# Performance work log

Hardware: AMD Instinct MI355X
Metric: run time of the kernel (lower is better)

Reference implementation:

```python
import jax, jax.numpy as jnp
import numpy as np

N_NODES = 100000
N_EDGES = 1600000
IN_DIM = 128
HID_DIM = 128


def _gcn_conv(x, edge_index, W, b, num_nodes):
    h = x @ W  # [N, H]
    loops = jnp.arange(num_nodes, dtype=edge_index.dtype)
    src = jnp.concatenate([edge_index[0], loops])  # [E+N]
    dst = jnp.concatenate([edge_index[1], loops])
    deg = jax.ops.segment_sum(jnp.ones_like(dst, dtype=h.dtype), dst,
                              num_segments=num_nodes)  # [N], >=1 due to self-loops
    inv_sqrt_deg = jax.lax.rsqrt(deg)
    norm = inv_sqrt_deg[src] * inv_sqrt_deg[dst]  # [E+N]
    msgs = h[src] * norm[:, None]  # gather + scale, [E+N, H]
    out = jax.ops.segment_sum(msgs, dst, num_segments=num_nodes)  # scatter-add
    return out + b


def setup_inputs() -> dict:
    key = jax.random.key(0)
    k1, k2, k3, k4, k5 = jax.random.split(key, 5)
    x = jax.random.normal(k1, (N_NODES, IN_DIM), dtype=jnp.float32)
    edge_index = jax.random.randint(k2, (2, N_EDGES), 0, N_NODES, dtype=jnp.int64)
    s1 = 1.0 / np.sqrt(IN_DIM)
    s2 = 1.0 / np.sqrt(HID_DIM)
    W1 = jax.random.uniform(k3, (IN_DIM, HID_DIM), jnp.float32, -s1, s1)
    W2 = jax.random.uniform(k4, (HID_DIM, HID_DIM), jnp.float32, -s2, s2)
    b1 = jnp.zeros((HID_DIM,), jnp.float32)
    b2 = jnp.zeros((HID_DIM,), jnp.float32)
    return {"x": x, "edge_index": edge_index, "W1": W1, "b1": b1, "W2": W2, "b2": b2}


def reference(x, edge_index, W1, b1, W2, b2):
    n = x.shape[0]
    h = _gcn_conv(x, edge_index, W1, b1, n)
    h = jax.nn.relu(h)
    h = _gcn_conv(h, edge_index, W2, b2, n)
    return h.mean(axis=0)  # [HID_DIM]
```

## Files before the change

### kernel.cpp

```cpp
#include <hip/hip_runtime.h>

#define TPB 256

typedef unsigned int uint32;
typedef float float4v __attribute__((ext_vector_type(4)));
typedef unsigned int uint4v __attribute__((ext_vector_type(4)));

static __device__ __forceinline__ unsigned short f2bf(float f) {
  unsigned int u = __float_as_uint(f);
  unsigned int r = (u + 0x7FFFu + ((u >> 16) & 1u)) >> 16;
  return (unsigned short)r;
}
static __device__ __forceinline__ float bf_lo(uint32 v) {
  return __uint_as_float(v << 16);
}
static __device__ __forceinline__ float bf_hi(uint32 v) {
  return __uint_as_float(v & 0xFFFF0000u);
}

static __device__ __forceinline__ int edge_val(const int* __restrict__ ep,
                                               long long idx, int is64) {
  return is64 ? ep[2 * idx] : ep[idx];
}

__global__ void k_detect(const int* __restrict__ ep, long long E,
                         int* __restrict__ flag) {
  int lim = (E < 16384) ? (int)E : 16384;
  int found = 0;
  for (int i = threadIdx.x; i < lim; i += TPB) found |= (ep[2 * i + 1] != 0);
  if (found) atomicOr(flag, 1);
}

__global__ void k_count(const int* __restrict__ ep, long long E,
                        const int* __restrict__ flag, int* __restrict__ deg) {
  int is64 = (*flag == 0);
  long long stride = (long long)gridDim.x * blockDim.x;
  for (long long e = blockIdx.x * (long long)blockDim.x + threadIdx.x; e < E;
       e += stride) {
    int d = edge_val(ep, E + e, is64);
    atomicAdd(&deg[d], 1);
  }
}

__global__ void k_bsum(const int* __restrict__ deg, int N,
                       int* __restrict__ bsums) {
  __shared__ int lds[TPB];
  int t = threadIdx.x;
  int i = blockIdx.x * TPB + t;
  lds[t] = (i < N) ? deg[i] : 0;
  __syncthreads();
  for (int off = TPB / 2; off > 0; off >>= 1) {
    if (t < off) lds[t] += lds[t + off];
    __syncthreads();
  }
  if (t == 0) bsums[blockIdx.x] = lds[0];
}

__global__ void k_bscan(int* __restrict__ bsums, int nb) {
  __shared__ int lds[512];
  int t = threadIdx.x;
  int v = (t < nb) ? bsums[t] : 0;
  lds[t] = v;
  __syncthreads();
  for (int off = 1; off < 512; off <<= 1) {
    int x = (t >= off) ? lds[t - off] : 0;
    __syncthreads();
    lds[t] += x;
    __syncthreads();
  }
  if (t < nb) bsums[t] = lds[t] - v;
}

__global__ void k_scan3(const int* __restrict__ deg, const int* __restrict__ bsums,
                        int N, int* __restrict__ row_start, int* __restrict__ cursor,
                        float* __restrict__ r) {
  __shared__ int lds[TPB];
  int t = threadIdx.x;
  int i = blockIdx.x * TPB + t;
  int v = (i < N) ? deg[i] : 0;
  lds[t] = v;
  __syncthreads();
  for (int off = 1; off < TPB; off <<= 1) {
    int x = (t >= off) ? lds[t - off] : 0;
    __syncthreads();
    lds[t] += x;
    __syncthreads();
  }
  if (i < N) {
    int ex = lds[t] - v + bsums[blockIdx.x];
    row_start[i] = ex;
    cursor[i] = ex;
    r[i] = rsqrtf((float)(v + 1));
  }
}

__global__ void k_fill(const int* __restrict__ ep, long long E,
                       const int* __restrict__ flag, int* __restrict__ cursor,
                       int* __restrict__ csr_src) {
  int is64 = (*flag == 0);
  long long stride = (long long)gridDim.x * blockDim.x;
  for (long long e = blockIdx.x * (long long)blockDim.x + threadIdx.x; e < E;
       e += stride) {
    int s = edge_val(ep, e, is64);
    int d = edge_val(ep, E + e, is64);
    int pos = atomicAdd(&cursor[d], 1);
    csr_src[pos] = s;
  }
}

template <int XBF>
__global__ __launch_bounds__(TPB, 4) void k_gemm(
    const void* __restrict__ Xv, const float* __restrict__ W,
    const float* __restrict__ r, unsigned short* __restrict__ outB, int N) {
  __shared__ uint32 wl[128 * 64];
  for (int i = threadIdx.x; i < 128 * 64; i += TPB) {
    int k = i >> 6, p = i & 63;
    float2 wv = *reinterpret_cast<const float2*>(&W[k * 128 + p * 2]);
    wl[i] = (uint32)f2bf(wv.x) | ((uint32)f2bf(wv.y) << 16);
  }
  __syncthreads();
  int wave = threadIdx.x >> 6, lane = threadIdx.x & 63;
  int row0 = (blockIdx.x * 4 + wave) * 8;
  if (row0 >= N) return;
  const int c0 = lane * 2;
  float2 acc[8];
#pragma unroll
  for (int q = 0; q < 8; q++) acc[q] = make_float2(0.f, 0.f);

  if (XBF == 0) {
    const float* X = (const float*)Xv;
    for (int kk = 0; kk < 128; kk += 4) {
      float4v xv[8];
#pragma unroll
      for (int q = 0; q < 8; q++) {
        int rr = row0 + q;
        if (rr >= N) rr = N - 1;
        xv[q] = __builtin_nontemporal_load(
            reinterpret_cast<const float4v*>(&X[(size_t)rr * 128 + kk]));
      }
#pragma unroll
      for (int u = 0; u < 4; u++) {
        uint32 wv = wl[(kk + u) * 64 + lane];
        float wx = bf_lo(wv), wy = bf_hi(wv);
#pragma unroll
        for (int q = 0; q < 8; q++) {
          float xk = xv[q][u];
          acc[q].x = fmaf(xk, wx, acc[q].x);
          acc[q].y = fmaf(xk, wy, acc[q].y);
        }
      }
    }
  } else {
    const unsigned short* X = (const unsigned short*)Xv;
    for (int kk = 0; kk < 128; kk += 8) {
      uint4v xv[8];
#pragma unroll
      for (int q = 0; q < 8; q++) {
        int rr = row0 + q;
        if (rr >= N) rr = N - 1;
        xv[q] = *reinterpret_cast<const uint4v*>(&X[(size_t)rr * 128 + kk]);
      }
#pragma unroll
      for (int u = 0; u < 8; u++) {
        uint32 wv = wl[(kk + u) * 64 + lane];
        float wx = bf_lo(wv), wy = bf_hi(wv);
#pragma unroll
        for (int q = 0; q < 8; q++) {
          uint32 xw = xv[q][u >> 1];
          float xk = (u & 1) ? bf_hi(xw) : bf_lo(xw);
          acc[q].x = fmaf(xk, wx, acc[q].x);
          acc[q].y = fmaf(xk, wy, acc[q].y);
        }
      }
    }
  }
#pragma unroll
  for (int q = 0; q < 8; q++) {
    int rr = row0 + q;
    if (rr < N) {
      float sc = r[rr];
      uint32 o = (uint32)f2bf(acc[q].x * sc) | ((uint32)f2bf(acc[q].y * sc) << 16);
      *reinterpret_cast<uint32*>(&outB[(size_t)rr * 128 + c0]) = o;
    }
  }
}

template <int RELU, int COLSUM>
__global__ __launch_bounds__(TPB) void k_agg(
    const unsigned short* __restrict__ HsB, const float* __restrict__ r,
    const int* __restrict__ row_start, const int* __restrict__ deg,
    const int* __restrict__ csr_src, const float* __restrict__ bias,
    unsigned short* __restrict__ outB, float* __restrict__ colsum, int N) {
  __shared__ float red[4][128];
  int wave = threadIdx.x >> 6, lane = threadIdx.x & 63;
  int gw = blockIdx.x * 4 + wave, nw = gridDim.x * 4;
  const int c0 = lane * 2;
  float2 b = *reinterpret_cast<const float2*>(&bias[c0]);
  float2 csum = make_float2(0.f, 0.f);

  for (int i0 = gw; i0 < N; i0 += 2 * nw) {
    const int iA = i0;
    const int iB = i0 + nw;
    const int hasB = (iB < N);
    int sA = __builtin_amdgcn_readfirstlane(row_start[iA]);
    int dA = __builtin_amdgcn_readfirstlane(deg[iA]);
    int sB = 0, dB = 0;
    if (hasB) {
      sB = __builtin_amdgcn_readfirstlane(row_start[iB]);
      dB = __builtin_amdgcn_readfirstlane(deg[iB]);
    }
    uint32 selfA = *reinterpret_cast<const uint32*>(&HsB[(size_t)iA * 128 + c0]);
    float2 aA = make_float2(bf_lo(selfA), bf_hi(selfA));
    float2 aB = make_float2(0.f, 0.f);
    if (hasB) {
      uint32 selfB = *reinterpret_cast<const uint32*>(&HsB[(size_t)iB * 128 + c0]);
      aB = make_float2(bf_lo(selfB), bf_hi(selfB));
    }
    int jA = 0, jB = 0;
    while (jA + 8 <= dA && jB + 8 <= dB) {
      int ia[8], ib[8];
#pragma unroll
      for (int u = 0; u < 8; u++) ia[u] = csr_src[sA + jA + u];
#pragma unroll
      for (int u = 0; u < 8; u++) ib[u] = csr_src[sB + jB + u];
      uint32 va[8], vb[8];
#pragma unroll
      for (int u = 0; u < 8; u++)
        va[u] = *reinterpret_cast<const uint32*>(&HsB[(size_t)ia[u] * 128 + c0]);
#pragma unroll
      for (int u = 0; u < 8; u++)
        vb[u] = *reinterpret_cast<const uint32*>(&HsB[(size_t)ib[u] * 128 + c0]);
#pragma unroll
      for (int u = 0; u < 8; u++) {
        aA.x += bf_lo(va[u]); aA.y += bf_hi(va[u]);
        aB.x += bf_lo(vb[u]); aB.y += bf_hi(vb[u]);
      }
      jA += 8; jB += 8;
    }
    while (jA + 8 <= dA) {
      int ia[8];
#pragma unroll
      for (int u = 0; u < 8; u++) ia[u] = csr_src[sA + jA + u];
      uint32 va[8];
#pragma unroll
      for (int u = 0; u < 8; u++)
        va[u] = *reinterpret_cast<const uint32*>(&HsB[(size_t)ia[u] * 128 + c0]);
#pragma unroll
      for (int u = 0; u < 8; u++) { aA.x += bf_lo(va[u]); aA.y += bf_hi(va[u]); }
      jA += 8;
    }
    while (jB + 8 <= dB) {
      int ib[8];
#pragma unroll
      for (int u = 0; u < 8; u++) ib[u] = csr_src[sB + jB + u];
      uint32 vb[8];
#pragma unroll
      for (int u = 0; u < 8; u++)
        vb[u] = *reinterpret_cast<const uint32*>(&HsB[(size_t)ib[u] * 128 + c0]);
#pragma unroll
      for (int u = 0; u < 8; u++) { aB.x += bf_lo(vb[u]); aB.y += bf_hi(vb[u]); }
      jB += 8;
    }
    if (jA + 4 <= dA && jB + 4 <= dB) {
      int ia[4], ib[4];
#pragma unroll
      for (int u = 0; u < 4; u++) ia[u] = csr_src[sA + jA + u];
#pragma unroll
      for (int u = 0; u < 4; u++) ib[u] = csr_src[sB + jB + u];
      uint32 va[4], vb[4];
#pragma unroll
      for (int u = 0; u < 4; u++)
        va[u] = *reinterpret_cast<const uint32*>(&HsB[(size_t)ia[u] * 128 + c0]);
#pragma unroll
      for (int u = 0; u < 4; u++)
        vb[u] = *reinterpret_cast<const uint32*>(&HsB[(size_t)ib[u] * 128 + c0]);
#pragma unroll
      for (int u = 0; u < 4; u++) {
        aA.x += bf_lo(va[u]); aA.y += bf_hi(va[u]);
        aB.x += bf_lo(vb[u]); aB.y += bf_hi(vb[u]);
      }
      jA += 4; jB += 4;
    }
    if (jA + 4 <= dA) {
      int ia[4];
#pragma unroll
      for (int u = 0; u < 4; u++) ia[u] = csr_src[sA + jA + u];
      uint32 va[4];
#pragma unroll
      for (int u = 0; u < 4; u++)
        va[u] = *reinterpret_cast<const uint32*>(&HsB[(size_t)ia[u] * 128 + c0]);
#pragma unroll
      for (int u = 0; u < 4; u++) { aA.x += bf_lo(va[u]); aA.y += bf_hi(va[u]); }
      jA += 4;
    }
    if (jB + 4 <= dB) {
      int ib[4];
#pragma unroll
      for (int u = 0; u < 4; u++) ib[u] = csr_src[sB + jB + u];
      uint32 vb[4];
#pragma unroll
      for (int u = 0; u < 4; u++)
        vb[u] = *reinterpret_cast<const uint32*>(&HsB[(size_t)ib[u] * 128 + c0]);
#pragma unroll
      for (int u = 0; u < 4; u++) { aB.x += bf_lo(vb[u]); aB.y += bf_hi(vb[u]); }
      jB += 4;
    }
    for (; jA < dA && jB < dB; jA++, jB++) {
      int s0 = csr_src[sA + jA], s1 = csr_src[sB + jB];
      uint32 v0 = *reinterpret_cast<const uint32*>(&HsB[(size_t)s0 * 128 + c0]);
      uint32 v1 = *reinterpret_cast<const uint32*>(&HsB[(size_t)s1 * 128 + c0]);
      aA.x += bf_lo(v0); aA.y += bf_hi(v0);
      aB.x += bf_lo(v1); aB.y += bf_hi(v1);
    }
    for (; jA < dA; jA++) {
      int s0 = csr_src[sA + jA];
      uint32 v0 = *reinterpret_cast<const uint32*>(&HsB[(size_t)s0 * 128 + c0]);
      aA.x += bf_lo(v0); aA.y += bf_hi(v0);
    }
    for (; jB < dB; jB++) {
      int s1 = csr_src[sB + jB];
      uint32 v1 = *reinterpret_cast<const uint32*>(&HsB[(size_t)s1 * 128 + c0]);
      aB.x += bf_lo(v1); aB.y += bf_hi(v1);
    }
    {
      float ri = r[iA];
      float v0 = fmaf(ri, aA.x, b.x), v1 = fmaf(ri, aA.y, b.y);
      if (RELU) { v0 = fmaxf(v0, 0.f); v1 = fmaxf(v1, 0.f); }
      if (COLSUM) {
        csum.x += v0; csum.y += v1;
      } else {
        uint32 o = (uint32)f2bf(v0) | ((uint32)f2bf(v1) << 16);
        __builtin_nontemporal_store(
            o, reinterpret_cast<uint32*>(&outB[(size_t)iA * 128 + c0]));
      }
    }
    if (hasB) {
      float ri = r[iB];
      float v0 = fmaf(ri, aB.x, b.x), v1 = fmaf(ri, aB.y, b.y);
      if (RELU) { v0 = fmaxf(v0, 0.f); v1 = fmaxf(v1, 0.f); }
      if (COLSUM) {
        csum.x += v0; csum.y += v1;
      } else {
        uint32 o = (uint32)f2bf(v0) | ((uint32)f2bf(v1) << 16);
        __builtin_nontemporal_store(
            o, reinterpret_cast<uint32*>(&outB[(size_t)iB * 128 + c0]));
      }
    }
  }
  if (COLSUM) {
    red[wave][c0] = csum.x;
    red[wave][c0 + 1] = csum.y;
    __syncthreads();
    if (wave == 0) {
      float sx = red[0][c0] + red[1][c0] + red[2][c0] + red[3][c0];
      float sy = red[0][c0 + 1] + red[1][c0 + 1] + red[2][c0 + 1] + red[3][c0 + 1];
      atomicAdd(&colsum[c0], sx);
      atomicAdd(&colsum[c0 + 1], sy);
    }
  }
}

__global__ void k_final(const float* __restrict__ colsum, float* __restrict__ out,
                        float invN) {
  int c = threadIdx.x;
  out[c] = colsum[c] * invN;
}

extern "C" void kernel_launch(void* const* d_in, const int* in_sizes, int n_in,
                              void* d_out, int out_size, void* d_ws, size_t ws_size,
                              hipStream_t stream) {
  const float* x = (const float*)d_in[0];
  const int* ep = (const int*)d_in[1];
  const float* W1 = (const float*)d_in[2];
  const float* b1 = (const float*)d_in[3];
  const float* W2 = (const float*)d_in[4];
  const float* b2 = (const float*)d_in[5];
  float* outp = (float*)d_out;

  const int N = in_sizes[0] / 128;
  const long long E = in_sizes[1] / 2;

  char* ws = (char*)d_ws;
  size_t off = 0;
  auto carve = [&](size_t bytes) -> void* {
    void* p = ws + off;
    off = (off + bytes + 255) & ~(size_t)255;
    return p;
  };
  unsigned short* HsB = (unsigned short*)carve((size_t)N * 128 * 2);
  unsigned short* YB = (unsigned short*)carve((size_t)N * 128 * 2);
  float* rr = (float*)carve((size_t)N * 4);
  int* deg = (int*)carve((size_t)N * 4);
  int* rs = (int*)carve((size_t)N * 4);
  int* cur = (int*)carve((size_t)N * 4);
  int* csr = (int*)carve((size_t)E * 4);
  int* bsums = (int*)carve(4096 * 4);
  int* flag = (int*)carve(256);
  float* colsum = (float*)carve(512);

  hipMemsetAsync(flag, 0, 4, stream);
  hipMemsetAsync(deg, 0, (size_t)N * 4, stream);
  hipMemsetAsync(colsum, 0, 512, stream);

  k_detect<<<1, TPB, 0, stream>>>(ep, E, flag);
  k_count<<<2048, TPB, 0, stream>>>(ep, E, flag, deg);
  int nb = (N + TPB - 1) / TPB;
  k_bsum<<<nb, TPB, 0, stream>>>(deg, N, bsums);
  k_bscan<<<1, 512, 0, stream>>>(bsums, nb);
  k_scan3<<<nb, TPB, 0, stream>>>(deg, bsums, N, rs, cur, rr);
  k_fill<<<2048, TPB, 0, stream>>>(ep, E, flag, cur, csr);

  int gblocks = (N + 31) / 32;
  k_gemm<0><<<gblocks, TPB, 0, stream>>>(x, W1, rr, HsB, N);
  k_agg<1, 0><<<2048, TPB, 0, stream>>>(HsB, rr, rs, deg, csr, b1, YB, nullptr, N);
  k_gemm<1><<<gblocks, TPB, 0, stream>>>(YB, W2, rr, HsB, N);
  k_agg<0, 1><<<2048, TPB, 0, stream>>>(HsB, rr, rs, deg, csr, b2, nullptr, colsum, N);
  k_final<<<1, 128, 0, stream>>>(colsum, outp, 1.0f / (float)N);
}
```

Baseline: 744.0 us.

## Fuse second-layer GEMM into first aggregation kernel epilogue

The layer-1 aggregation kernel now multiplies each finished row by W2, held as bf16 in shared memory, and writes the scaled layer-2 features directly. This removes the separate second GEMM launch and the bf16 round trip of the intermediate activations. The cost is a per-row 128x128 matvec done by one wave through LDS, which is less efficient than a tiled GEMM and adds 32KB of LDS per block, which can lower occupancy of the latency-bound gather. It also splits the aggregation into two specialized kernels and makes the CSR fill use nontemporal stores.

New measurement: 997.6 us. +34.1%, slower.

```diff
diff --git a/kernel.cpp b/kernel.cpp
--- a/kernel.cpp
+++ b/kernel.cpp
@@ -104,13 +104,12 @@
     int s = edge_val(ep, e, is64);
     int d = edge_val(ep, E + e, is64);
     int pos = atomicAdd(&cursor[d], 1);
-    csr_src[pos] = s;
-  }
-}
-
-template <int XBF>
+    __builtin_nontemporal_store(s, &csr_src[pos]);
+  }
+}
+
 __global__ __launch_bounds__(TPB, 4) void k_gemm(
-    const void* __restrict__ Xv, const float* __restrict__ W,
+    const float* __restrict__ X, const float* __restrict__ W,
     const float* __restrict__ r, unsigned short* __restrict__ outB, int N) {
   __shared__ uint32 wl[128 * 64];
   for (int i = threadIdx.x; i < 128 * 64; i += TPB) {
@@ -126,51 +125,24 @@
   float2 acc[8];
 #pragma unroll
   for (int q = 0; q < 8; q++) acc[q] = make_float2(0.f, 0.f);
-
-  if (XBF == 0) {
-    const float* X = (const float*)Xv;
-    for (int kk = 0; kk < 128; kk += 4) {
-      float4v xv[8];
+  for (int kk = 0; kk < 128; kk += 4) {
+    float4v xv[8];
+#pragma unroll
+    for (int q = 0; q < 8; q++) {
+      int rr = row0 + q;
+      if (rr >= N) rr = N - 1;
+      xv[q] = __builtin_nontemporal_load(
+          reinterpret_cast<const float4v*>(&X[(size_t)rr * 128 + kk]));
+    }
+#pragma unroll
+    for (int u = 0; u < 4; u++) {
+      uint32 wv = wl[(kk + u) * 64 + lane];
+      float wx = bf_lo(wv), wy = bf_hi(wv);
 #pragma unroll
       for (int q = 0; q < 8; q++) {
-        int rr = row0 + q;
-        if (rr >= N) rr = N - 1;
-        xv[q] = __builtin_nontemporal_load(
-            reinterpret_cast<const float4v*>(&X[(size_t)rr * 128 + kk]));
-      }
-#pragma unroll
-      for (int u = 0; u < 4; u++) {
-        uint32 wv = wl[(kk + u) * 64 + lane];
-        float wx = bf_lo(wv), wy = bf_hi(wv);
-#pragma unroll
-        for (int q = 0; q < 8; q++) {
-          float xk = xv[q][u];
-          acc[q].x = fmaf(xk, wx, acc[q].x);
-          acc[q].y = fmaf(xk, wy, acc[q].y);
-        }
-      }
-    }
-  } else {
-    const unsigned short* X = (const unsigned short*)Xv;
-    for (int kk = 0; kk < 128; kk += 8) {
-      uint4v xv[8];
-#pragma unroll
-      for (int q = 0; q < 8; q++) {
-        int rr = row0 + q;
-        if (rr >= N) rr = N - 1;
-        xv[q] = *reinterpret_cast<const uint4v*>(&X[(size_t)rr * 128 + kk]);
-      }
-#pragma unroll
-      for (int u = 0; u < 8; u++) {
-        uint32 wv = wl[(kk + u) * 64 + lane];
-        float wx = bf_lo(wv), wy = bf_hi(wv);
-#pragma unroll
-        for (int q = 0; q < 8; q++) {
-          uint32 xw = xv[q][u >> 1];
-          float xk = (u & 1) ? bf_hi(xw) : bf_lo(xw);
-          acc[q].x = fmaf(xk, wx, acc[q].x);
-          acc[q].y = fmaf(xk, wy, acc[q].y);
-        }
+        float xk = xv[q][u];
+        acc[q].x = fmaf(xk, wx, acc[q].x);
+        acc[q].y = fmaf(xk, wy, acc[q].y);
       }
     }
   }
@@ -185,18 +157,43 @@
   }
 }
 
-template <int RELU, int COLSUM>
-__global__ __launch_bounds__(TPB) void k_agg(
+static __device__ __forceinline__ void y_to_hs2(
+    float v0, float v1, float ri, int i, int wave, int lane, int c0,
+    const uint32* __restrict__ w2l, float* __restrict__ yrow,
+    unsigned short* __restrict__ outB) {
+  float* yw = yrow + wave * 128;
+  *reinterpret_cast<float2*>(&yw[lane * 2]) = make_float2(v0, v1);
+  float hx = 0.f, hy = 0.f;
+  for (int k4 = 0; k4 < 32; k4++) {
+    float4v y4 = *reinterpret_cast<const float4v*>(&yw[k4 * 4]);
+#pragma unroll
+    for (int j = 0; j < 4; j++) {
+      uint32 wv = w2l[(k4 * 4 + j) * 64 + lane];
+      hx = fmaf(y4[j], bf_lo(wv), hx);
+      hy = fmaf(y4[j], bf_hi(wv), hy);
+    }
+  }
+  uint32 o = (uint32)f2bf(hx * ri) | ((uint32)f2bf(hy * ri) << 16);
+  *reinterpret_cast<uint32*>(&outB[(size_t)i * 128 + c0]) = o;
+}
+
+__global__ __launch_bounds__(TPB) void k_aggF(
     const unsigned short* __restrict__ HsB, const float* __restrict__ r,
     const int* __restrict__ row_start, const int* __restrict__ deg,
     const int* __restrict__ csr_src, const float* __restrict__ bias,
-    unsigned short* __restrict__ outB, float* __restrict__ colsum, int N) {
-  __shared__ float red[4][128];
+    const float* __restrict__ W2, unsigned short* __restrict__ outB, int N) {
+  __shared__ uint32 w2l[128 * 64];
+  __shared__ float yrow[4 * 128];
+  for (int i = threadIdx.x; i < 128 * 64; i += TPB) {
+    int k = i >> 6, p = i & 63;
+    float2 wv = *reinterpret_cast<const float2*>(&W2[k * 128 + p * 2]);
+    w2l[i] = (uint32)f2bf(wv.x) | ((uint32)f2bf(wv.y) << 16);
+  }
+  __syncthreads();
   int wave = threadIdx.x >> 6, lane = threadIdx.x & 63;
   int gw = blockIdx.x * 4 + wave, nw = gridDim.x * 4;
   const int c0 = lane * 2;
   float2 b = *reinterpret_cast<const float2*>(&bias[c0]);
-  float2 csum = make_float2(0.f, 0.f);
 
   for (int i0 = gw; i0 < N; i0 += 2 * nw) {
     const int iA = i0;
@@ -325,38 +322,173 @@
     {
       float ri = r[iA];
       float v0 = fmaf(ri, aA.x, b.x), v1 = fmaf(ri, aA.y, b.y);
-      if (RELU) { v0 = fmaxf(v0, 0.f); v1 = fmaxf(v1, 0.f); }
-      if (COLSUM) {
-        csum.x += v0; csum.y += v1;
-      } else {
-        uint32 o = (uint32)f2bf(v0) | ((uint32)f2bf(v1) << 16);
-        __builtin_nontemporal_store(
-            o, reinterpret_cast<uint32*>(&outB[(size_t)iA * 128 + c0]));
-      }
+      v0 = fmaxf(v0, 0.f); v1 = fmaxf(v1, 0.f);
+      y_to_hs2(v0, v1, ri, iA, wave, lane, c0, w2l, yrow, outB);
     }
     if (hasB) {
       float ri = r[iB];
       float v0 = fmaf(ri, aB.x, b.x), v1 = fmaf(ri, aB.y, b.y);
-      if (RELU) { v0 = fmaxf(v0, 0.f); v1 = fmaxf(v1, 0.f); }
-      if (COLSUM) {
-        csum.x += v0; csum.y += v1;
-      } else {
-        uint32 o = (uint32)f2bf(v0) | ((uint32)f2bf(v1) << 16);
-        __builtin_nontemporal_store(
-            o, reinterpret_cast<uint32*>(&outB[(size_t)iB * 128 + c0]));
+      v0 = fmaxf(v0, 0.f); v1 = fmaxf(v1, 0.f);
+      y_to_hs2(v0, v1, ri, iB, wave, lane, c0, w2l, yrow, outB);
+    }
+  }
+}
+
+__global__ __launch_bounds__(TPB) void k_aggS(
+    const unsigned short* __restrict__ HsB, const float* __restrict__ r,
+    const int* __restrict__ row_start, const int* __restrict__ deg,
+    const int* __restrict__ csr_src, const float* __restrict__ bias,
+    float* __restrict__ colsum, int N) {
+  __shared__ float red[4][128];
+  int wave = threadIdx.x >> 6, lane = threadIdx.x & 63;
+  int gw = blockIdx.x * 4 + wave, nw = gridDim.x * 4;
+  const int c0 = lane * 2;
+  float2 b = *reinterpret_cast<const float2*>(&bias[c0]);
+  float2 csum = make_float2(0.f, 0.f);
+
+  for (int i0 = gw; i0 < N; i0 += 2 * nw) {
+    const int iA = i0;
+    const int iB = i0 + nw;
+    const int hasB = (iB < N);
+    int sA = __builtin_amdgcn_readfirstlane(row_start[iA]);
+    int dA = __builtin_amdgcn_readfirstlane(deg[iA]);
+    int sB = 0, dB = 0;
+    if (hasB) {
+      sB = __builtin_amdgcn_readfirstlane(row_start[iB]);
+      dB = __builtin_amdgcn_readfirstlane(deg[iB]);
+    }
+    uint32 selfA = *reinterpret_cast<const uint32*>(&HsB[(size_t)iA * 128 + c0]);
+    float2 aA = make_float2(bf_lo(selfA), bf_hi(selfA));
+    float2 aB = make_float2(0.f, 0.f);
+    if (hasB) {
+      uint32 selfB = *reinterpret_cast<const uint32*>(&HsB[(size_t)iB * 128 + c0]);
+      aB = make_float2(bf_lo(selfB), bf_hi(selfB));
+    }
+    int jA = 0, jB = 0;
+    while (jA + 8 <= dA && jB + 8 <= dB) {
+      int ia[8], ib[8];
+#pragma unroll
+      for (int u = 0; u < 8; u++) ia[u] = csr_src[sA + jA + u];
+#pragma unroll
+      for (int u = 0; u < 8; u++) ib[u] = csr_src[sB + jB + u];
+      uint32 va[8], vb[8];
+#pragma unroll
+      for (int u = 0; u < 8; u++)
+        va[u] = *reinterpret_cast<const uint32*>(&HsB[(size_t)ia[u] * 128 + c0]);
+#pragma unroll
+      for (int u = 0; u < 8; u++)
+        vb[u] = *reinterpret_cast<const uint32*>(&HsB[(size_t)ib[u] * 128 + c0]);
+#pragma unroll
+      for (int u = 0; u < 8; u++) {
+        aA.x += bf_lo(va[u]); aA.y += bf_hi(va[u]);
+        aB.x += bf_lo(vb[u]); aB.y += bf_hi(vb[u]);
       }
-    }
-  }
-  if (COLSUM) {
-    red[wave][c0] = csum.x;
-    red[wave][c0 + 1] = csum.y;
-    __syncthreads();
-    if (wave == 0) {
-      float sx = red[0][c0] + red[1][c0] + red[2][c0] + red[3][c0];
-      float sy = red[0][c0 + 1] + red[1][c0 + 1] + red[2][c0 + 1] + red[3][c0 + 1];
-      atomicAdd(&colsum[c0], sx);
-      atomicAdd(&colsum[c0 + 1], sy);
-    }
+      jA += 8; jB += 8;
+    }
+    while (jA + 8 <= dA) {
+      int ia[8];
+#pragma unroll
+      for (int u = 0; u < 8; u++) ia[u] = csr_src[sA + jA + u];
+      uint32 va[8];
+#pragma unroll
+      for (int u = 0; u < 8; u++)
+        va[u] = *reinterpret_cast<const uint32*>(&HsB[(size_t)ia[u] * 128 + c0]);
+#pragma unroll
+      for (int u = 0; u < 8; u++) { aA.x += bf_lo(va[u]); aA.y += bf_hi(va[u]); }
+      jA += 8;
+    }
+    while (jB + 8 <= dB) {
+      int ib[8];
+#pragma unroll
+      for (int u = 0; u < 8; u++) ib[u] = csr_src[sB + jB + u];
+      uint32 vb[8];
+#pragma unroll
+      for (int u = 0; u < 8; u++)
+        vb[u] = *reinterpret_cast<const uint32*>(&HsB[(size_t)ib[u] * 128 + c0]);
+#pragma unroll
+      for (int u = 0; u < 8; u++) { aB.x += bf_lo(vb[u]); aB.y += bf_hi(vb[u]); }
+      jB += 8;
+    }
+    if (jA + 4 <= dA && jB + 4 <= dB) {
+      int ia[4], ib[4];
+#pragma unroll
+      for (int u = 0; u < 4; u++) ia[u] = csr_src[sA + jA + u];
+#pragma unroll
+      for (int u = 0; u < 4; u++) ib[u] = csr_src[sB + jB + u];
+      uint32 va[4], vb[4];
+#pragma unroll
+      for (int u = 0; u < 4; u++)
+        va[u] = *reinterpret_cast<const uint32*>(&HsB[(size_t)ia[u] * 128 + c0]);
+#pragma unroll
+      for (int u = 0; u < 4; u++)
+        vb[u] = *reinterpret_cast<const uint32*>(&HsB[(size_t)ib[u] * 128 + c0]);
+#pragma unroll
+      for (int u = 0; u < 4; u++) {
+        aA.x += bf_lo(va[u]); aA.y += bf_hi(va[u]);
+        aB.x += bf_lo(vb[u]); aB.y += bf_hi(vb[u]);
+      }
+      jA += 4; jB += 4;
+    }
+    if (jA + 4 <= dA) {
+      int ia[4];
+#pragma unroll
+      for (int u = 0; u < 4; u++) ia[u] = csr_src[sA + jA + u];
+      uint32 va[4];
+#pragma unroll
+      for (int u = 0; u < 4; u++)
+        va[u] = *reinterpret_cast<const uint32*>(&HsB[(size_t)ia[u] * 128 + c0]);
+#pragma unroll
+      for (int u = 0; u < 4; u++) { aA.x += bf_lo(va[u]); aA.y += bf_hi(va[u]); }
+      jA += 4;
+    }
+    if (jB + 4 <= dB) {
+      int ib[4];
+#pragma unroll
+      for (int u = 0; u < 4; u++) ib[u] = csr_src[sB + jB + u];
+      uint32 vb[4];
+#pragma unroll
+      for (int u = 0; u < 4; u++)
+        vb[u] = *reinterpret_cast<const uint32*>(&HsB[(size_t)ib[u] * 128 + c0]);
+#pragma unroll
+      for (int u = 0; u < 4; u++) { aB.x += bf_lo(vb[u]); aB.y += bf_hi(vb[u]); }
+      jB += 4;
+    }
+    for (; jA < dA && jB < dB; jA++, jB++) {
+      int s0 = csr_src[sA + jA], s1 = csr_src[sB + jB];
+      uint32 v0 = *reinterpret_cast<const uint32*>(&HsB[(size_t)s0 * 128 + c0]);
+      uint32 v1 = *reinterpret_cast<const uint32*>(&HsB[(size_t)s1 * 128 + c0]);
+      aA.x += bf_lo(v0); aA.y += bf_hi(v0);
+      aB.x += bf_lo(v1); aB.y += bf_hi(v1);
+    }
+    for (; jA < dA; jA++) {
+      int s0 = csr_src[sA + jA];
+      uint32 v0 = *reinterpret_cast<const uint32*>(&HsB[(size_t)s0 * 128 + c0]);
+      aA.x += bf_lo(v0); aA.y += bf_hi(v0);
+    }
+    for (; jB < dB; jB++) {
+      int s1 = csr_src[sB + jB];
+      uint32 v1 = *reinterpret_cast<const uint32*>(&HsB[(size_t)s1 * 128 + c0]);
+      aB.x += bf_lo(v1); aB.y += bf_hi(v1);
+    }
+    {
+      float ri = r[iA];
+      csum.x += fmaf(ri, aA.x, b.x);
+      csum.y += fmaf(ri, aA.y, b.y);
+    }
+    if (hasB) {
+      float ri = r[iB];
+      csum.x += fmaf(ri, aB.x, b.x);
+      csum.y += fmaf(ri, aB.y, b.y);
+    }
+  }
+  red[wave][c0] = csum.x;
+  red[wave][c0 + 1] = csum.y;
+  __syncthreads();
+  if (wave == 0) {
+    float sx = red[0][c0] + red[1][c0] + red[2][c0] + red[3][c0];
+    float sy = red[0][c0 + 1] + red[1][c0 + 1] + red[2][c0 + 1] + red[3][c0 + 1];
+    atomicAdd(&colsum[c0], sx);
+    atomicAdd(&colsum[c0 + 1], sy);
   }
 }
 
@@ -388,7 +520,7 @@
     return p;
   };
   unsigned short* HsB = (unsigned short*)carve((size_t)N * 128 * 2);
-  unsigned short* YB = (unsigned short*)carve((size_t)N * 128 * 2);
+  unsigned short* Hs2B = (unsigned short*)carve((size_t)N * 128 * 2);
   float* rr = (float*)carve((size_t)N * 4);
   int* deg = (int*)carve((size_t)N * 4);
   int* rs = (int*)carve((size_t)N * 4);
@@ -411,9 +543,8 @@
   k_fill<<<2048, TPB, 0, stream>>>(ep, E, flag, cur, csr);
 
   int gblocks = (N + 31) / 32;
-  k_gemm<0><<<gblocks, TPB, 0, stream>>>(x, W1, rr, HsB, N);
-  k_agg<1, 0><<<2048, TPB, 0, stream>>>(HsB, rr, rs, deg, csr, b1, YB, nullptr, N);
-  k_gemm<1><<<gblocks, TPB, 0, stream>>>(YB, W2, rr, HsB, N);
-  k_agg<0, 1><<<2048, TPB, 0, stream>>>(HsB, rr, rs, deg, csr, b2, nullptr, colsum, N);
+  k_gemm<<<gblocks, TPB, 0, stream>>>(x, W1, rr, HsB, N);
+  k_aggF<<<2048, TPB, 0, stream>>>(HsB, rr, rs, deg, csr, b1, W2, Hs2B, N);
+  k_aggS<<<2048, TPB, 0, stream>>>(Hs2B, rr, rs, deg, csr, b2, colsum, N);
   k_final<<<1, 128, 0, stream>>>(colsum, outp, 1.0f / (float)N);
 }
```
